# Optimization experiments

Hardware: AMD Instinct MI355X
Metric: run time of the kernel (lower is better)

## Reference

```python
import jax, jax.numpy as jnp
import numpy as np

N = 100_000   # nodes
E = 1_600_000 # edges
F = 128       # num_features
H = 128       # hidden
L = 3         # num_conv_layers
G = 512       # graphs in batch
BN_EPS = 1e-5


def _xavier(key, shape):
    fan_in, fan_out = shape[-1], shape[-2]
    scale = jnp.sqrt(2.0 / (fan_in + fan_out))
    return jax.random.normal(key, shape, dtype=jnp.float32) * scale


def setup_inputs() -> dict:
    key = jax.random.key(0)
    ks = jax.random.split(key, 10)
    x = jax.random.normal(ks[0], (N, F), dtype=jnp.float32)
    edge_index = jax.random.randint(ks[1], (2, E), 0, N, dtype=jnp.int32)
    batch = jnp.sort(jax.random.randint(ks[2], (N,), 0, G, dtype=jnp.int32))
    return {
        "x": x,
        "edge_index": edge_index,
        "batch": batch,
        "t1_w": _xavier(ks[3], (H, F)),
        "t1_b": jnp.zeros((H,), jnp.float32),
        "t2_w": _xavier(ks[4], (H, H)),
        "t2_b": jnp.zeros((H,), jnp.float32),
        "W1": _xavier(ks[5], (L, H, H)),
        "b1": jnp.zeros((L, H), jnp.float32),
        "gamma": jnp.ones((L, H), jnp.float32),
        "beta": jnp.zeros((L, H), jnp.float32),
        "W2": _xavier(ks[6], (L, H, H)),
        "b2": jnp.zeros((L, H), jnp.float32),
    }


def reference(x, edge_index, batch, t1_w, t1_b, t2_w, t2_b, W1, b1, gamma, beta, W2, b2):
    src, dst = edge_index[0], edge_index[1]
    # input transform (dropout is identity in eval mode)
    h = jax.nn.relu(x @ t1_w.T + t1_b)  # [N, H]
    # BN eval mode: running_mean=0, running_var=1 -> affine scale only
    bn_scale = gamma * jax.lax.rsqrt(jnp.float32(1.0 + BN_EPS))  # [L, H]
    for l in range(L):
        # GINConv with eps=0: (1+eps)*h_i + sum_{j->i} h_j
        agg = jax.ops.segment_sum(h[src], dst, num_segments=N)  # [N, H]
        z = h + agg
        z = z @ W1[l].T + b1[l]
        z = z * bn_scale[l] + beta[l]
        z = jax.nn.relu(z)
        h = z @ W2[l].T + b2[l]
    h = h @ t2_w.T + t2_b  # [N, H]
    graph_emb = jax.ops.segment_sum(h, batch, num_segments=G)  # [G, H]
    return graph_emb
```

## Files before the change

kernel.cpp:

```cpp
#include <hip/hip_runtime.h>
#include <hip/hip_bf16.h>

#define NNODES 100000
#define NEDGES 1600000
#define NR     100096
#define NGRAPH 512
#define NB     782
#define NBLK_BIN 128
#define EPB    12500

typedef __attribute__((ext_vector_type(8))) __bf16 bf16x8;
typedef __attribute__((ext_vector_type(4))) float f32x4;
typedef __attribute__((ext_vector_type(4))) unsigned int u32x4;
typedef __attribute__((ext_vector_type(2))) unsigned int u32x2;

__device__ __forceinline__ float b2f(unsigned int u16) {
    union { float f; unsigned int i; } v; v.i = (u16 & 0xffffu) << 16; return v.f;
}
__device__ __forceinline__ unsigned short f2b(float f) {
    union { float f; unsigned int i; } v; v.f = f;
    unsigned int u = (v.i + 0x7fffu + ((v.i >> 16) & 1u)) >> 16;
    return (unsigned short)u;
}

__global__ __launch_bounds__(256) void wconv(const float* __restrict__ t1w,
                                             const float* __restrict__ t2w,
                                             const float* __restrict__ W1,
                                             const float* __restrict__ W2,
                                             unsigned short* __restrict__ Wb) {
    int i = blockIdx.x * 256 + threadIdx.x;
    float4 v;
    if (i < 4096)       v = reinterpret_cast<const float4*>(t1w)[i];
    else if (i < 8192)  v = reinterpret_cast<const float4*>(t2w)[i - 4096];
    else if (i < 20480) v = reinterpret_cast<const float4*>(W1)[i - 8192];
    else                v = reinterpret_cast<const float4*>(W2)[i - 20480];
    u32x2 o;
    o.x = (unsigned int)f2b(v.x) | ((unsigned int)f2b(v.y) << 16);
    o.y = (unsigned int)f2b(v.z) | ((unsigned int)f2b(v.w) << 16);
    *reinterpret_cast<u32x2*>(Wb + (size_t)i * 4) = o;
}

__global__ __launch_bounds__(256) void hist_k(const int* __restrict__ dst,
                                              int* __restrict__ ghist) {
    __shared__ int lh[NB];
    int blk = blockIdx.x, tid = threadIdx.x;
    for (int i = tid; i < NB; i += 256) lh[i] = 0;
    __syncthreads();
    int s = blk * EPB;
    for (int i = s + tid; i < s + EPB; i += 256) atomicAdd(&lh[dst[i] >> 7], 1);
    __syncthreads();
    for (int b = tid; b < NB; b += 256) ghist[b * NBLK_BIN + blk] = lh[b];
}

__global__ __launch_bounds__(256) void scan_pairs(const int* __restrict__ ghist,
                                                  int* __restrict__ off,
                                                  int* __restrict__ tot) {
    int wid = threadIdx.x >> 6, lane = threadIdx.x & 63;
    int b = blockIdx.x * 4 + wid;
    if (b >= NB) return;
    int v0 = ghist[b * NBLK_BIN + lane * 2];
    int v1 = ghist[b * NBLK_BIN + lane * 2 + 1];
    int s = v0 + v1, incl = s;
    for (int o = 1; o < 64; o <<= 1) {
        int t = __shfl_up(incl, o);
        if (lane >= o) incl += t;
    }
    int excl = incl - s;
    off[b * NBLK_BIN + lane * 2] = excl;
    off[b * NBLK_BIN + lane * 2 + 1] = excl + v0;
    if (lane == 63) tot[b] = incl;
}

__global__ __launch_bounds__(1024) void boff_scan(const int* __restrict__ tot,
                                                  int* __restrict__ boff) {
    __shared__ int sm[1024];
    int t = threadIdx.x;
    int v = (t < NB) ? tot[t] : 0;
    sm[t] = v;
    __syncthreads();
    for (int o = 1; o < 1024; o <<= 1) {
        int u = (t >= o) ? sm[t - o] : 0;
        __syncthreads();
        sm[t] += u;
        __syncthreads();
    }
    if (t < NB) boff[t] = sm[t] - v;
    if (t == NB - 1) boff[NB] = sm[t];
}

__global__ __launch_bounds__(256) void scatter2(const int* __restrict__ src,
                                                const int* __restrict__ dst,
                                                const int* __restrict__ off,
                                                const int* __restrict__ boff,
                                                unsigned int* __restrict__ binned) {
    __shared__ int lbase[NB];
    __shared__ int lcnt[NB];
    int blk = blockIdx.x, tid = threadIdx.x;
    for (int b = tid; b < NB; b += 256) {
        lbase[b] = boff[b] + off[b * NBLK_BIN + blk];
        lcnt[b] = 0;
    }
    __syncthreads();
    int s0 = blk * EPB;
    for (int i = s0 + tid; i < s0 + EPB; i += 256) {
        int d = dst[i];
        int b = d >> 7;
        int r = atomicAdd(&lcnt[b], 1);
        binned[lbase[b] + r] = (unsigned int)src[i] | ((unsigned int)(d & 127) << 17);
    }
}

__global__ __launch_bounds__(256) void csr_build(const int* __restrict__ boff,
                                                 const unsigned int* __restrict__ binned,
                                                 int* __restrict__ rowptr,
                                                 int* __restrict__ csr) {
    __shared__ int lhist[128], lscan[128], lcnt[128];
    int b = blockIdx.x, tid = threadIdx.x;
    int s = boff[b], e = boff[b + 1];
    if (tid < 128) { lhist[tid] = 0; lcnt[tid] = 0; }
    __syncthreads();
    for (int i = s + tid; i < e; i += 256)
        atomicAdd(&lhist[(binned[i] >> 17) & 127], 1);
    __syncthreads();
    if (tid < 128) lscan[tid] = lhist[tid];
    __syncthreads();
    for (int o = 1; o < 128; o <<= 1) {
        int v = (tid < 128 && tid >= o) ? lscan[tid - o] : 0;
        __syncthreads();
        if (tid < 128) lscan[tid] += v;
        __syncthreads();
    }
    if (tid < 128) {
        int n = b * 128 + tid;
        if (n <= NNODES) rowptr[n] = s + lscan[tid] - lhist[tid];
    }
    __syncthreads();
    for (int i = s + tid; i < e; i += 256) {
        unsigned int v = binned[i];
        int dl = (v >> 17) & 127;
        int r = atomicAdd(&lcnt[dl], 1);
        csr[s + lscan[dl] - lhist[dl] + r] = (int)(v & 0x1FFFFu);
    }
}

__global__ __launch_bounds__(256) void agg_node4(const unsigned short* __restrict__ hb,
                                                 const int* __restrict__ rowptr,
                                                 const int* __restrict__ csr,
                                                 unsigned short* __restrict__ zb) {
    int wid = threadIdx.x >> 6, lane = threadIdx.x & 63;
    int node = blockIdx.x * 4 + wid;
    if (node >= NNODES) return;
    const int g  = lane >> 4;
    const int fl = lane & 15;

    float a0 = 0.f, a1 = 0.f, a2 = 0.f, a3 = 0.f, a4 = 0.f, a5 = 0.f, a6 = 0.f, a7 = 0.f;
    const int s = rowptr[node], e = rowptr[node + 1];

    int i = s + g;
    for (; i + 12 < e; i += 16) {
        int j0 = csr[i];
        int j1 = csr[i + 4];
        int j2 = csr[i + 8];
        int j3 = csr[i + 12];
        u32x4 v0 = *reinterpret_cast<const u32x4*>(hb + (size_t)j0 * 128 + fl * 8);
        u32x4 v1 = *reinterpret_cast<const u32x4*>(hb + (size_t)j1 * 128 + fl * 8);
        u32x4 v2 = *reinterpret_cast<const u32x4*>(hb + (size_t)j2 * 128 + fl * 8);
        u32x4 v3 = *reinterpret_cast<const u32x4*>(hb + (size_t)j3 * 128 + fl * 8);
        a0 += b2f(v0.x); a1 += b2f(v0.x >> 16);
        a2 += b2f(v0.y); a3 += b2f(v0.y >> 16);
        a4 += b2f(v0.z); a5 += b2f(v0.z >> 16);
        a6 += b2f(v0.w); a7 += b2f(v0.w >> 16);
        a0 += b2f(v1.x); a1 += b2f(v1.x >> 16);
        a2 += b2f(v1.y); a3 += b2f(v1.y >> 16);
        a4 += b2f(v1.z); a5 += b2f(v1.z >> 16);
        a6 += b2f(v1.w); a7 += b2f(v1.w >> 16);
        a0 += b2f(v2.x); a1 += b2f(v2.x >> 16);
        a2 += b2f(v2.y); a3 += b2f(v2.y >> 16);
        a4 += b2f(v2.z); a5 += b2f(v2.z >> 16);
        a6 += b2f(v2.w); a7 += b2f(v2.w >> 16);
        a0 += b2f(v3.x); a1 += b2f(v3.x >> 16);
        a2 += b2f(v3.y); a3 += b2f(v3.y >> 16);
        a4 += b2f(v3.z); a5 += b2f(v3.z >> 16);
        a6 += b2f(v3.w); a7 += b2f(v3.w >> 16);
    }
    for (; i < e; i += 4) {
        int j0 = csr[i];
        u32x4 v0 = *reinterpret_cast<const u32x4*>(hb + (size_t)j0 * 128 + fl * 8);
        a0 += b2f(v0.x); a1 += b2f(v0.x >> 16);
        a2 += b2f(v0.y); a3 += b2f(v0.y >> 16);
        a4 += b2f(v0.z); a5 += b2f(v0.z >> 16);
        a6 += b2f(v0.w); a7 += b2f(v0.w >> 16);
    }

    a0 += __shfl_xor(a0, 16); a1 += __shfl_xor(a1, 16);
    a2 += __shfl_xor(a2, 16); a3 += __shfl_xor(a3, 16);
    a4 += __shfl_xor(a4, 16); a5 += __shfl_xor(a5, 16);
    a6 += __shfl_xor(a6, 16); a7 += __shfl_xor(a7, 16);
    a0 += __shfl_xor(a0, 32); a1 += __shfl_xor(a1, 32);
    a2 += __shfl_xor(a2, 32); a3 += __shfl_xor(a3, 32);
    a4 += __shfl_xor(a4, 32); a5 += __shfl_xor(a5, 32);
    a6 += __shfl_xor(a6, 32); a7 += __shfl_xor(a7, 32);

    if (g == 0) {
        u32x4 sv = *reinterpret_cast<const u32x4*>(hb + (size_t)node * 128 + fl * 8);
        a0 += b2f(sv.x); a1 += b2f(sv.x >> 16);
        a2 += b2f(sv.y); a3 += b2f(sv.y >> 16);
        a4 += b2f(sv.z); a5 += b2f(sv.z >> 16);
        a6 += b2f(sv.w); a7 += b2f(sv.w >> 16);
        u32x4 o;
        o.x = (unsigned int)f2b(a0) | ((unsigned int)f2b(a1) << 16);
        o.y = (unsigned int)f2b(a2) | ((unsigned int)f2b(a3) << 16);
        o.z = (unsigned int)f2b(a4) | ((unsigned int)f2b(a5) << 16);
        o.w = (unsigned int)f2b(a6) | ((unsigned int)f2b(a7) << 16);
        *reinterpret_cast<u32x4*>(zb + (size_t)node * 128 + fl * 8) = o;
    }
}

template <int SRC_F32, int MODE>
__global__ __launch_bounds__(256) void gemm128(const void* __restrict__ Asrc, int src_rows,
                                               const unsigned short* __restrict__ Wb,
                                               const float* __restrict__ bias,
                                               const float* __restrict__ gamma,
                                               const float* __restrict__ beta,
                                               unsigned short* __restrict__ Out) {
    __shared__ unsigned short lsA[128 * 128];
    __shared__ unsigned short lsB[128 * 128];
    const int tid = threadIdx.x;
    const int blockRow = blockIdx.x * 128;

    for (int it = 0; it < 8; ++it) {
        int idx = it * 256 + tid;
        int row = idx >> 4;
        int u = idx & 15;
        uint4 v = *reinterpret_cast<const uint4*>(Wb + (size_t)row * 128 + u * 8);
        int boffb = row * 256 + ((u * 16) ^ ((row & 7) << 4));
        *reinterpret_cast<uint4*>((char*)lsB + boffb) = v;
    }
    if (SRC_F32) {
        const float* A = (const float*)Asrc;
        for (int it = 0; it < 16; ++it) {
            int fidx = it * 256 + tid;
            int row = fidx >> 5;
            int c4 = (fidx & 31) * 4;
            int gr = blockRow + row; if (gr > src_rows - 1) gr = src_rows - 1;
            float4 v = *reinterpret_cast<const float4*>(A + (size_t)gr * 128 + c4);
            int boffb = row * 256 + ((c4 * 2) ^ ((row & 7) << 4));
            unsigned short* p = (unsigned short*)((char*)lsA + boffb);
            p[0] = f2b(v.x); p[1] = f2b(v.y); p[2] = f2b(v.z); p[3] = f2b(v.w);
        }
    } else {
        const unsigned short* A = (const unsigned short*)Asrc;
        for (int it = 0; it < 8; ++it) {
            int idx = it * 256 + tid;
            int row = idx >> 4;
            int u = idx & 15;
            int gr = blockRow + row;
            uint4 v = *reinterpret_cast<const uint4*>(A + (size_t)gr * 128 + u * 8);
            int boffb = row * 256 + ((u * 16) ^ ((row & 7) << 4));
            *reinterpret_cast<uint4*>((char*)lsA + boffb) = v;
        }
    }
    __syncthreads();

    const int lane = tid & 63;
    const int w = tid >> 6;
    const int wr = w >> 1, wc = w & 1;

    f32x4 acc[4][4];
    f32x4 zv = {0.f, 0.f, 0.f, 0.f};
#pragma unroll
    for (int m = 0; m < 4; ++m)
#pragma unroll
        for (int n = 0; n < 4; ++n) acc[m][n] = zv;

#pragma unroll
    for (int ks = 0; ks < 4; ++ks) {
        int kbb = ks * 64 + ((lane >> 4) << 4);
        bf16x8 af[4], bfr[4];
#pragma unroll
        for (int m = 0; m < 4; ++m) {
            int ar = wr * 64 + m * 16 + (lane & 15);
            af[m] = *reinterpret_cast<const bf16x8*>((char*)lsA + ar * 256 + (kbb ^ ((ar & 7) << 4)));
        }
#pragma unroll
        for (int n = 0; n < 4; ++n) {
            int bc = wc * 64 + n * 16 + (lane & 15);
            bfr[n] = *reinterpret_cast<const bf16x8*>((char*)lsB + bc * 256 + (kbb ^ ((bc & 7) << 4)));
        }
#pragma unroll
        for (int m = 0; m < 4; ++m)
#pragma unroll
            for (int n = 0; n < 4; ++n)
                acc[m][n] = __builtin_amdgcn_mfma_f32_16x16x32_bf16(af[m], bfr[n], acc[m][n], 0, 0, 0);
    }

#pragma unroll
    for (int n = 0; n < 4; ++n) {
        int col = wc * 64 + n * 16 + (lane & 15);
        float bb = bias[col];
        float sc = 1.f, bt = 0.f;
        if (MODE == 2) { sc = gamma[col] * rsqrtf(1.0f + 1e-5f); bt = beta[col]; }
#pragma unroll
        for (int m = 0; m < 4; ++m) {
            int r0 = blockRow + wr * 64 + m * 16 + ((lane >> 4) << 2);
#pragma unroll
            for (int r = 0; r < 4; ++r) {
                float v = acc[m][n][r] + bb;
                if (MODE == 2) v = v * sc + bt;
                if (MODE >= 1) v = fmaxf(v, 0.f);
                Out[(size_t)(r0 + r) * 128 + col] = f2b(v);
            }
        }
    }
}

__global__ __launch_bounds__(128) void segsum(const unsigned short* __restrict__ hf,
                                              const int* __restrict__ batch,
                                              float* __restrict__ out) {
    int g = blockIdx.x, f = threadIdx.x;
    int lo = 0, hi = NNODES;
    while (lo < hi) { int mid = (lo + hi) >> 1; if (batch[mid] < g) lo = mid + 1; else hi = mid; }
    int s = lo;
    lo = 0; hi = NNODES;
    while (lo < hi) { int mid = (lo + hi) >> 1; if (batch[mid] < g + 1) lo = mid + 1; else hi = mid; }
    int e = lo;
    float acc0 = 0.f, acc1 = 0.f, acc2 = 0.f, acc3 = 0.f;
    int n = s;
    for (; n + 3 < e; n += 4) {
        acc0 += b2f(hf[(size_t)n * 128 + f]);
        acc1 += b2f(hf[(size_t)(n + 1) * 128 + f]);
        acc2 += b2f(hf[(size_t)(n + 2) * 128 + f]);
        acc3 += b2f(hf[(size_t)(n + 3) * 128 + f]);
    }
    for (; n < e; ++n) acc0 += b2f(hf[(size_t)n * 128 + f]);
    out[(size_t)g * 128 + f] = (acc0 + acc1) + (acc2 + acc3);
}

extern "C" void kernel_launch(void* const* d_in, const int* in_sizes, int n_in,
                              void* d_out, int out_size, void* d_ws, size_t ws_size,
                              hipStream_t stream) {
    const float* x     = (const float*)d_in[0];
    const int*   ei    = (const int*)d_in[1];
    const int*   batch = (const int*)d_in[2];
    const float* t1w   = (const float*)d_in[3];
    const float* t1b   = (const float*)d_in[4];
    const float* t2w   = (const float*)d_in[5];
    const float* t2b   = (const float*)d_in[6];
    const float* W1    = (const float*)d_in[7];
    const float* b1    = (const float*)d_in[8];
    const float* gamma = (const float*)d_in[9];
    const float* beta  = (const float*)d_in[10];
    const float* W2    = (const float*)d_in[11];
    const float* b2    = (const float*)d_in[12];
    float* out = (float*)d_out;

    char* ws = (char*)d_ws;
    size_t off_b = 0;
    auto alloc = [&](size_t bytes) -> void* {
        off_b = (off_b + 511) & ~size_t(511);
        void* p = ws + off_b;
        off_b += bytes;
        return p;
    };
    unsigned short* hbA = (unsigned short*)alloc((size_t)NR * 128 * 2);
    unsigned short* zb  = (unsigned short*)alloc((size_t)NR * 128 * 2);
    unsigned short* Wb  = (unsigned short*)alloc((size_t)131072 * 2);
    int* rowptr         = (int*)alloc((size_t)(NNODES + 2) * 4);
    int* ghist          = (int*)alloc((size_t)NB * NBLK_BIN * 4);
    int* off            = (int*)alloc((size_t)NB * NBLK_BIN * 4);
    int* tot            = (int*)alloc((size_t)NB * 4);
    int* boff           = (int*)alloc((size_t)(NB + 1) * 4);
    unsigned int* binned = (unsigned int*)alloc((size_t)NEDGES * 4);
    int* csr            = (int*)alloc((size_t)NEDGES * 4);

    const int* esrc = ei;
    const int* edst = ei + NEDGES;

    wconv<<<128, 256, 0, stream>>>(t1w, t2w, W1, W2, Wb);

    hist_k<<<NBLK_BIN, 256, 0, stream>>>(edst, ghist);
    scan_pairs<<<(NB + 3) / 4, 256, 0, stream>>>(ghist, off, tot);
    boff_scan<<<1, 1024, 0, stream>>>(tot, boff);
    scatter2<<<NBLK_BIN, 256, 0, stream>>>(esrc, edst, off, boff, binned);
    csr_build<<<NB, 256, 0, stream>>>(boff, binned, rowptr, csr);

    gemm128<1, 1><<<NR / 128, 256, 0, stream>>>(x, NNODES, Wb, t1b, nullptr, nullptr, hbA);

    for (int l = 0; l < 3; ++l) {
        agg_node4<<<25000, 256, 0, stream>>>(hbA, rowptr, csr, zb);
        gemm128<0, 2><<<NR / 128, 256, 0, stream>>>(zb, NR, Wb + 32768 + (size_t)l * 16384,
                                                    b1 + l * 128, gamma + l * 128, beta + l * 128,
                                                    zb);
        gemm128<0, 0><<<NR / 128, 256, 0, stream>>>(zb, NR, Wb + 81920 + (size_t)l * 16384,
                                                    b2 + l * 128, nullptr, nullptr, hbA);
    }
    gemm128<0, 0><<<NR / 128, 256, 0, stream>>>(hbA, NR, Wb + 16384, t2b, nullptr, nullptr, zb);
    segsum<<<NGRAPH, 128, 0, stream>>>(zb, batch, out);
}
```

Baseline: 489.8 us.

## Fuse aggregation and both MLP GEMMs into one per-layer kernel

```diff
diff --git a/kernel.cpp b/kernel.cpp
--- a/kernel.cpp
+++ b/kernel.cpp
@@ -143,76 +143,191 @@
     }
 }
 
-__global__ __launch_bounds__(256) void agg_node4(const unsigned short* __restrict__ hb,
-                                                 const int* __restrict__ rowptr,
-                                                 const int* __restrict__ csr,
-                                                 unsigned short* __restrict__ zb) {
-    int wid = threadIdx.x >> 6, lane = threadIdx.x & 63;
-    int node = blockIdx.x * 4 + wid;
-    if (node >= NNODES) return;
+__global__ __launch_bounds__(512) void layer_fused(const unsigned short* __restrict__ hPrev,
+                                                   const int* __restrict__ rowptr,
+                                                   const int* __restrict__ csr,
+                                                   const unsigned short* __restrict__ W1b,
+                                                   const unsigned short* __restrict__ W2b,
+                                                   const float* __restrict__ b1,
+                                                   const float* __restrict__ gamma,
+                                                   const float* __restrict__ beta,
+                                                   const float* __restrict__ b2,
+                                                   unsigned short* __restrict__ hNext) {
+    __shared__ unsigned short lsZ[128 * 128];
+    __shared__ unsigned short lsB[128 * 128];
+    const int tid = threadIdx.x;
+    const int w = tid >> 6;
+    const int lane = tid & 63;
+    const int nodeBase = blockIdx.x * 128;
     const int g  = lane >> 4;
     const int fl = lane & 15;
 
-    float a0 = 0.f, a1 = 0.f, a2 = 0.f, a3 = 0.f, a4 = 0.f, a5 = 0.f, a6 = 0.f, a7 = 0.f;
-    const int s = rowptr[node], e = rowptr[node + 1];
-
-    int i = s + g;
-    for (; i + 12 < e; i += 16) {
-        int j0 = csr[i];
-        int j1 = csr[i + 4];
-        int j2 = csr[i + 8];
-        int j3 = csr[i + 12];
-        u32x4 v0 = *reinterpret_cast<const u32x4*>(hb + (size_t)j0 * 128 + fl * 8);
-        u32x4 v1 = *reinterpret_cast<const u32x4*>(hb + (size_t)j1 * 128 + fl * 8);
-        u32x4 v2 = *reinterpret_cast<const u32x4*>(hb + (size_t)j2 * 128 + fl * 8);
-        u32x4 v3 = *reinterpret_cast<const u32x4*>(hb + (size_t)j3 * 128 + fl * 8);
-        a0 += b2f(v0.x); a1 += b2f(v0.x >> 16);
-        a2 += b2f(v0.y); a3 += b2f(v0.y >> 16);
-        a4 += b2f(v0.z); a5 += b2f(v0.z >> 16);
-        a6 += b2f(v0.w); a7 += b2f(v0.w >> 16);
-        a0 += b2f(v1.x); a1 += b2f(v1.x >> 16);
-        a2 += b2f(v1.y); a3 += b2f(v1.y >> 16);
-        a4 += b2f(v1.z); a5 += b2f(v1.z >> 16);
-        a6 += b2f(v1.w); a7 += b2f(v1.w >> 16);
-        a0 += b2f(v2.x); a1 += b2f(v2.x >> 16);
-        a2 += b2f(v2.y); a3 += b2f(v2.y >> 16);
-        a4 += b2f(v2.z); a5 += b2f(v2.z >> 16);
-        a6 += b2f(v2.w); a7 += b2f(v2.w >> 16);
-        a0 += b2f(v3.x); a1 += b2f(v3.x >> 16);
-        a2 += b2f(v3.y); a3 += b2f(v3.y >> 16);
-        a4 += b2f(v3.z); a5 += b2f(v3.z >> 16);
-        a6 += b2f(v3.w); a7 += b2f(v3.w >> 16);
-    }
-    for (; i < e; i += 4) {
-        int j0 = csr[i];
-        u32x4 v0 = *reinterpret_cast<const u32x4*>(hb + (size_t)j0 * 128 + fl * 8);
-        a0 += b2f(v0.x); a1 += b2f(v0.x >> 16);
-        a2 += b2f(v0.y); a3 += b2f(v0.y >> 16);
-        a4 += b2f(v0.z); a5 += b2f(v0.z >> 16);
-        a6 += b2f(v0.w); a7 += b2f(v0.w >> 16);
-    }
-
-    a0 += __shfl_xor(a0, 16); a1 += __shfl_xor(a1, 16);
-    a2 += __shfl_xor(a2, 16); a3 += __shfl_xor(a3, 16);
-    a4 += __shfl_xor(a4, 16); a5 += __shfl_xor(a5, 16);
-    a6 += __shfl_xor(a6, 16); a7 += __shfl_xor(a7, 16);
-    a0 += __shfl_xor(a0, 32); a1 += __shfl_xor(a1, 32);
-    a2 += __shfl_xor(a2, 32); a3 += __shfl_xor(a3, 32);
-    a4 += __shfl_xor(a4, 32); a5 += __shfl_xor(a5, 32);
-    a6 += __shfl_xor(a6, 32); a7 += __shfl_xor(a7, 32);
-
-    if (g == 0) {
-        u32x4 sv = *reinterpret_cast<const u32x4*>(hb + (size_t)node * 128 + fl * 8);
-        a0 += b2f(sv.x); a1 += b2f(sv.x >> 16);
-        a2 += b2f(sv.y); a3 += b2f(sv.y >> 16);
-        a4 += b2f(sv.z); a5 += b2f(sv.z >> 16);
-        a6 += b2f(sv.w); a7 += b2f(sv.w >> 16);
-        u32x4 o;
-        o.x = (unsigned int)f2b(a0) | ((unsigned int)f2b(a1) << 16);
-        o.y = (unsigned int)f2b(a2) | ((unsigned int)f2b(a3) << 16);
-        o.z = (unsigned int)f2b(a4) | ((unsigned int)f2b(a5) << 16);
-        o.w = (unsigned int)f2b(a6) | ((unsigned int)f2b(a7) << 16);
-        *reinterpret_cast<u32x4*>(zb + (size_t)node * 128 + fl * 8) = o;
+#pragma unroll
+    for (int it = 0; it < 4; ++it) {
+        int idx = it * 512 + tid;
+        int row = idx >> 4, u = idx & 15;
+        uint4 v = *reinterpret_cast<const uint4*>(W1b + (size_t)row * 128 + u * 8);
+        *reinterpret_cast<uint4*>((char*)lsB + row * 256 + ((u * 16) ^ ((row & 7) << 4))) = v;
+    }
+
+    for (int nl = 0; nl < 16; ++nl) {
+        const int lr = w * 16 + nl;
+        const int node = nodeBase + lr;
+        float a0 = 0.f, a1 = 0.f, a2 = 0.f, a3 = 0.f, a4 = 0.f, a5 = 0.f, a6 = 0.f, a7 = 0.f;
+        int s = 0, e = 0;
+        if (node < NNODES) { s = rowptr[node]; e = rowptr[node + 1]; }
+        int i = s + g;
+        for (; i + 12 < e; i += 16) {
+            int j0 = csr[i];
+            int j1 = csr[i + 4];
+            int j2 = csr[i + 8];
+            int j3 = csr[i + 12];
+            u32x4 v0 = *reinterpret_cast<const u32x4*>(hPrev + (size_t)j0 * 128 + fl * 8);
+            u32x4 v1 = *reinterpret_cast<const u32x4*>(hPrev + (size_t)j1 * 128 + fl * 8);
+            u32x4 v2 = *reinterpret_cast<const u32x4*>(hPrev + (size_t)j2 * 128 + fl * 8);
+            u32x4 v3 = *reinterpret_cast<const u32x4*>(hPrev + (size_t)j3 * 128 + fl * 8);
+            a0 += b2f(v0.x); a1 += b2f(v0.x >> 16);
+            a2 += b2f(v0.y); a3 += b2f(v0.y >> 16);
+            a4 += b2f(v0.z); a5 += b2f(v0.z >> 16);
+            a6 += b2f(v0.w); a7 += b2f(v0.w >> 16);
+            a0 += b2f(v1.x); a1 += b2f(v1.x >> 16);
+            a2 += b2f(v1.y); a3 += b2f(v1.y >> 16);
+            a4 += b2f(v1.z); a5 += b2f(v1.z >> 16);
+            a6 += b2f(v1.w); a7 += b2f(v1.w >> 16);
+            a0 += b2f(v2.x); a1 += b2f(v2.x >> 16);
+            a2 += b2f(v2.y); a3 += b2f(v2.y >> 16);
+            a4 += b2f(v2.z); a5 += b2f(v2.z >> 16);
+            a6 += b2f(v2.w); a7 += b2f(v2.w >> 16);
+            a0 += b2f(v3.x); a1 += b2f(v3.x >> 16);
+            a2 += b2f(v3.y); a3 += b2f(v3.y >> 16);
+            a4 += b2f(v3.z); a5 += b2f(v3.z >> 16);
+            a6 += b2f(v3.w); a7 += b2f(v3.w >> 16);
+        }
+        for (; i < e; i += 4) {
+            int j0 = csr[i];
+            u32x4 v0 = *reinterpret_cast<const u32x4*>(hPrev + (size_t)j0 * 128 + fl * 8);
+            a0 += b2f(v0.x); a1 += b2f(v0.x >> 16);
+            a2 += b2f(v0.y); a3 += b2f(v0.y >> 16);
+            a4 += b2f(v0.z); a5 += b2f(v0.z >> 16);
+            a6 += b2f(v0.w); a7 += b2f(v0.w >> 16);
+        }
+        a0 += __shfl_xor(a0, 16); a1 += __shfl_xor(a1, 16);
+        a2 += __shfl_xor(a2, 16); a3 += __shfl_xor(a3, 16);
+        a4 += __shfl_xor(a4, 16); a5 += __shfl_xor(a5, 16);
+        a6 += __shfl_xor(a6, 16); a7 += __shfl_xor(a7, 16);
+        a0 += __shfl_xor(a0, 32); a1 += __shfl_xor(a1, 32);
+        a2 += __shfl_xor(a2, 32); a3 += __shfl_xor(a3, 32);
+        a4 += __shfl_xor(a4, 32); a5 += __shfl_xor(a5, 32);
+        a6 += __shfl_xor(a6, 32); a7 += __shfl_xor(a7, 32);
+        if (g == 0) {
+            u32x4 sv = *reinterpret_cast<const u32x4*>(hPrev + (size_t)node * 128 + fl * 8);
+            a0 += b2f(sv.x); a1 += b2f(sv.x >> 16);
+            a2 += b2f(sv.y); a3 += b2f(sv.y >> 16);
+            a4 += b2f(sv.z); a5 += b2f(sv.z >> 16);
+            a6 += b2f(sv.w); a7 += b2f(sv.w >> 16);
+            u32x4 o;
+            o.x = (unsigned int)f2b(a0) | ((unsigned int)f2b(a1) << 16);
+            o.y = (unsigned int)f2b(a2) | ((unsigned int)f2b(a3) << 16);
+            o.z = (unsigned int)f2b(a4) | ((unsigned int)f2b(a5) << 16);
+            o.w = (unsigned int)f2b(a6) | ((unsigned int)f2b(a7) << 16);
+            *reinterpret_cast<u32x4*>((char*)lsZ + lr * 256 + ((fl * 16) ^ ((lr & 7) << 4))) = o;
+        }
+    }
+    __syncthreads();
+
+    const int wr = w >> 1, wc = w & 1;
+    f32x4 acc[2][4];
+    f32x4 zv = {0.f, 0.f, 0.f, 0.f};
+#pragma unroll
+    for (int m = 0; m < 2; ++m)
+#pragma unroll
+        for (int n = 0; n < 4; ++n) acc[m][n] = zv;
+#pragma unroll
+    for (int ks = 0; ks < 4; ++ks) {
+        int kbb = ks * 64 + ((lane >> 4) << 4);
+        bf16x8 af[2], bfr[4];
+#pragma unroll
+        for (int m = 0; m < 2; ++m) {
+            int ar = wr * 32 + m * 16 + (lane & 15);
+            af[m] = *reinterpret_cast<const bf16x8*>((char*)lsZ + ar * 256 + (kbb ^ ((ar & 7) << 4)));
+        }
+#pragma unroll
+        for (int n = 0; n < 4; ++n) {
+            int bc = wc * 64 + n * 16 + (lane & 15);
+            bfr[n] = *reinterpret_cast<const bf16x8*>((char*)lsB + bc * 256 + (kbb ^ ((bc & 7) << 4)));
+        }
+#pragma unroll
+        for (int m = 0; m < 2; ++m)
+#pragma unroll
+            for (int n = 0; n < 4; ++n)
+                acc[m][n] = __builtin_amdgcn_mfma_f32_16x16x32_bf16(af[m], bfr[n], acc[m][n], 0, 0, 0);
+    }
+    __syncthreads();
+
+#pragma unroll
+    for (int n = 0; n < 4; ++n) {
+        int col = wc * 64 + n * 16 + (lane & 15);
+        float bb = b1[col];
+        float sc = gamma[col] * rsqrtf(1.0f + 1e-5f);
+        float bt = beta[col];
+#pragma unroll
+        for (int m = 0; m < 2; ++m) {
+            int r0 = wr * 32 + m * 16 + ((lane >> 4) << 2);
+#pragma unroll
+            for (int r = 0; r < 4; ++r) {
+                float v = (acc[m][n][r] + bb) * sc + bt;
+                v = fmaxf(v, 0.f);
+                int row = r0 + r;
+                *(unsigned short*)((char*)lsZ + row * 256 + ((2 * col) ^ ((row & 7) << 4))) = f2b(v);
+            }
+        }
+    }
+#pragma unroll
+    for (int it = 0; it < 4; ++it) {
+        int idx = it * 512 + tid;
+        int row = idx >> 4, u = idx & 15;
+        uint4 v = *reinterpret_cast<const uint4*>(W2b + (size_t)row * 128 + u * 8);
+        *reinterpret_cast<uint4*>((char*)lsB + row * 256 + ((u * 16) ^ ((row & 7) << 4))) = v;
+    }
+    __syncthreads();
+
+    f32x4 acc2[2][4];
+#pragma unroll
+    for (int m = 0; m < 2; ++m)
+#pragma unroll
+        for (int n = 0; n < 4; ++n) acc2[m][n] = zv;
+#pragma unroll
+    for (int ks = 0; ks < 4; ++ks) {
+        int kbb = ks * 64 + ((lane >> 4) << 4);
+        bf16x8 af[2], bfr[4];
+#pragma unroll
+        for (int m = 0; m < 2; ++m) {
+            int ar = wr * 32 + m * 16 + (lane & 15);
+            af[m] = *reinterpret_cast<const bf16x8*>((char*)lsZ + ar * 256 + (kbb ^ ((ar & 7) << 4)));
+        }
+#pragma unroll
+        for (int n = 0; n < 4; ++n) {
+            int bc = wc * 64 + n * 16 + (lane & 15);
+            bfr[n] = *reinterpret_cast<const bf16x8*>((char*)lsB + bc * 256 + (kbb ^ ((bc & 7) << 4)));
+        }
+#pragma unroll
+        for (int m = 0; m < 2; ++m)
+#pragma unroll
+            for (int n = 0; n < 4; ++n)
+                acc2[m][n] = __builtin_amdgcn_mfma_f32_16x16x32_bf16(af[m], bfr[n], acc2[m][n], 0, 0, 0);
+    }
+
+#pragma unroll
+    for (int n = 0; n < 4; ++n) {
+        int col = wc * 64 + n * 16 + (lane & 15);
+        float bb = b2[col];
+#pragma unroll
+        for (int m = 0; m < 2; ++m) {
+            int r0 = nodeBase + wr * 32 + m * 16 + ((lane >> 4) << 2);
+#pragma unroll
+            for (int r = 0; r < 4; ++r)
+                hNext[(size_t)(r0 + r) * 128 + col] = f2b(acc2[m][n][r] + bb);
+        }
     }
 }
 
@@ -220,8 +335,6 @@
 __global__ __launch_bounds__(256) void gemm128(const void* __restrict__ Asrc, int src_rows,
                                                const unsigned short* __restrict__ Wb,
                                                const float* __restrict__ bias,
-                                               const float* __restrict__ gamma,
-                                               const float* __restrict__ beta,
                                                unsigned short* __restrict__ Out) {
     __shared__ unsigned short lsA[128 * 128];
     __shared__ unsigned short lsB[128 * 128];
@@ -298,15 +411,12 @@
     for (int n = 0; n < 4; ++n) {
         int col = wc * 64 + n * 16 + (lane & 15);
         float bb = bias[col];
-        float sc = 1.f, bt = 0.f;
-        if (MODE == 2) { sc = gamma[col] * rsqrtf(1.0f + 1e-5f); bt = beta[col]; }
 #pragma unroll
         for (int m = 0; m < 4; ++m) {
             int r0 = blockRow + wr * 64 + m * 16 + ((lane >> 4) << 2);
 #pragma unroll
             for (int r = 0; r < 4; ++r) {
                 float v = acc[m][n][r] + bb;
-                if (MODE == 2) v = v * sc + bt;
                 if (MODE >= 1) v = fmaxf(v, 0.f);
                 Out[(size_t)(r0 + r) * 128 + col] = f2b(v);
             }
@@ -363,7 +473,7 @@
         return p;
     };
     unsigned short* hbA = (unsigned short*)alloc((size_t)NR * 128 * 2);
-    unsigned short* zb  = (unsigned short*)alloc((size_t)NR * 128 * 2);
+    unsigned short* hbB = (unsigned short*)alloc((size_t)NR * 128 * 2);
     unsigned short* Wb  = (unsigned short*)alloc((size_t)131072 * 2);
     int* rowptr         = (int*)alloc((size_t)(NNODES + 2) * 4);
     int* ghist          = (int*)alloc((size_t)NB * NBLK_BIN * 4);
@@ -384,16 +494,18 @@
     scatter2<<<NBLK_BIN, 256, 0, stream>>>(esrc, edst, off, boff, binned);
     csr_build<<<NB, 256, 0, stream>>>(boff, binned, rowptr, csr);
 
-    gemm128<1, 1><<<NR / 128, 256, 0, stream>>>(x, NNODES, Wb, t1b, nullptr, nullptr, hbA);
-
+    gemm128<1, 1><<<NR / 128, 256, 0, stream>>>(x, NNODES, Wb, t1b, hbA);
+
+    const unsigned short* hin = hbA;
+    unsigned short* hout = hbB;
     for (int l = 0; l < 3; ++l) {
-        agg_node4<<<25000, 256, 0, stream>>>(hbA, rowptr, csr, zb);
-        gemm128<0, 2><<<NR / 128, 256, 0, stream>>>(zb, NR, Wb + 32768 + (size_t)l * 16384,
-                                                    b1 + l * 128, gamma + l * 128, beta + l * 128,
-                                                    zb);
-        gemm128<0, 0><<<NR / 128, 256, 0, stream>>>(zb, NR, Wb + 81920 + (size_t)l * 16384,
-                                                    b2 + l * 128, nullptr, nullptr, hbA);
-    }
-    gemm128<0, 0><<<NR / 128, 256, 0, stream>>>(hbA, NR, Wb + 16384, t2b, nullptr, nullptr, zb);
-    segsum<<<NGRAPH, 128, 0, stream>>>(zb, batch, out);
-}
+        layer_fused<<<NB, 512, 0, stream>>>(hin, rowptr, csr,
+                                            Wb + 32768 + (size_t)l * 16384,
+                                            Wb + 81920 + (size_t)l * 16384,
+                                            b1 + l * 128, gamma + l * 128, beta + l * 128,
+                                            b2 + l * 128, hout);
+        unsigned short* t = (unsigned short*)hin; hin = hout; hout = t;
+    }
+    gemm128<0, 0><<<NR / 128, 256, 0, stream>>>(hin, NR, Wb + 16384, t2b, hout);
+    segsum<<<NGRAPH, 128, 0, stream>>>(hout, batch, out);
+}
```

New measurement: 557.7 us. +13.9%, slower.
